# Performance work log

Measured on AMD Instinct MI355X. Metric: run time of the kernel, lower is better.

The kernel has to match this reference:

```python
import jax, jax.numpy as jnp
import numpy as np
from jax import lax

NUM_GROUPS = 16
POOL_K = 2
CLAMP_MIN = 0.0
CLAMP_MAX = 1.0
EPS = 1e-5


def setup_inputs() -> dict:
    key = jax.random.key(0)
    k1, k2, k3, k4, k5, k6 = jax.random.split(key, 6)
    B, Cin, H, W = 32, 64, 128, 128
    Cout, K = 128, 3
    x = jax.random.normal(k1, (B, Cin, H, W), dtype=jnp.float32)
    conv_w = jax.random.normal(k2, (Cout, Cin, K, K), dtype=jnp.float32) * 0.05
    conv_b = jax.random.normal(k3, (Cout,), dtype=jnp.float32) * 0.05
    gn_weight = jnp.ones((Cout,), dtype=jnp.float32) + 0.1 * jax.random.normal(k4, (Cout,), dtype=jnp.float32)
    gn_bias = 0.1 * jax.random.normal(k5, (Cout,), dtype=jnp.float32)
    scale = jnp.ones((Cout, 1, 1), dtype=jnp.float32) + 0.1 * jax.random.normal(k6, (Cout, 1, 1), dtype=jnp.float32)
    return {"x": x, "conv_w": conv_w, "conv_b": conv_b,
            "gn_weight": gn_weight, "gn_bias": gn_bias, "scale": scale}


def reference(x, conv_w, conv_b, gn_weight, gn_bias, scale):
    # Conv2d, VALID padding, stride 1  -> [B, C, H-2, W-2]
    y = lax.conv_general_dilated(
        x, conv_w, window_strides=(1, 1), padding='VALID',
        dimension_numbers=('NCHW', 'OIHW', 'NCHW'))
    y = y + conv_b[None, :, None, None]

    B, C, H, W = y.shape
    # GroupNorm: stats per (batch, group) over channels_per_group*H*W
    yg = y.reshape(B, NUM_GROUPS, -1)
    mean = jnp.mean(yg, axis=-1, keepdims=True)
    var = jnp.mean(jnp.square(yg - mean), axis=-1, keepdims=True)
    yn = ((yg - mean) * lax.rsqrt(var + EPS)).reshape(B, C, H, W)
    # affine + extra per-channel scale (fused elementwise)
    yn = (yn * gn_weight[None, :, None, None] + gn_bias[None, :, None, None]) * scale[None]

    # MaxPool2d(k=POOL_K), VALID, stride=k
    p = lax.reduce_window(yn, -jnp.inf, lax.max,
                          (1, 1, POOL_K, POOL_K), (1, 1, POOL_K, POOL_K), 'VALID')
    return jnp.clip(p, CLAMP_MIN, CLAMP_MAX)
```

## Files before the change

kernel.cpp:

```cpp
#include <hip/hip_runtime.h>

typedef _Float16 half8 __attribute__((ext_vector_type(8)));
typedef _Float16 half4t __attribute__((ext_vector_type(4)));
typedef _Float16 half2t __attribute__((ext_vector_type(2)));
typedef float float4t __attribute__((ext_vector_type(4)));
typedef float float4u __attribute__((ext_vector_type(4), aligned(4)));

#define BATCH 32
#define CIN 64
#define HIN 128
#define WIN 128
#define COUT 128
#define HOUT 126
#define WOUT 126
#define HP 63
#define WP 63
#define NGROUPS 16
#define CPG 8
#define EPSV 1e-5f

#define XPR 8320
#define XPRB 16640

__global__ __launch_bounds__(256) void wt_kernel(const float* __restrict__ w,
                                                 _Float16* __restrict__ wT) {
    int idx = blockIdx.x * 256 + threadIdx.x;
    if (idx >= 9 * COUT * CIN) return;
    int cin = idx & 63;
    int t = idx >> 6;
    int cout = t & 127;
    int pos = t >> 7;
    wT[idx] = (_Float16)w[(cout * CIN + cin) * 9 + pos];
}

__global__ __launch_bounds__(256) void repack_kernel(const float* __restrict__ x,
                                                     _Float16* __restrict__ xp) {
    __shared__ _Float16 lt[128 * 66];
    const int tid = threadIdx.x;
    const int grow = blockIdx.x;
    const int b = blockIdx.y;

    const int u = tid >> 5;
    const int col0 = (tid & 31) * 4;
    const float* xb = x + ((size_t)b * CIN * HIN + grow) * WIN;
#pragma unroll
    for (int i = 0; i < 4; i++) {
        int cin0 = 2 * (u + 8 * i);
        float4t va = *(const float4t*)(xb + (size_t)cin0 * HIN * WIN + col0);
        float4t vb = *(const float4t*)(xb + (size_t)(cin0 + 1) * HIN * WIN + col0);
#pragma unroll
        for (int j = 0; j < 4; j++) {
            half2t hv = { (_Float16)va[j], (_Float16)vb[j] };
            *(half2t*)&lt[(col0 + j) * 66 + cin0] = hv;
        }
    }
    __syncthreads();

    _Float16* xpb = xp + ((size_t)b * HIN + grow) * XPR;
#pragma unroll
    for (int k = 0; k < 16; k++) {
        int cidx = tid + 256 * k;
        int col = cidx >> 5, p = cidx & 31;
        half2t v = *(const half2t*)&lt[col * 66 + 2 * p];
        int slot = (p >> 2) ^ ((2 * grow + col) & 7);
        *(half2t*)(xpb + col * 64 + slot * 8 + (p & 3) * 2) = v;
    }
    if (tid < 16) {
        int col = 128 + (tid >> 3), chk = tid & 7;
        int slot = chk ^ ((2 * grow + col) & 7);
        half8 z;
#pragma unroll
        for (int j = 0; j < 8; j++) z[j] = (_Float16)0.f;
        *(half8*)(xpb + col * 64 + slot * 8) = z;
    }
}

__global__ __launch_bounds__(256, 2) void conv_mfma_kernel(
    const _Float16* __restrict__ xp, const _Float16* __restrict__ wT,
    const float* __restrict__ bias, unsigned int* __restrict__ pl,
    float* __restrict__ stats)
{
    __shared__ __align__(16) _Float16 xs[4 * XPR];

    const int tid = threadIdx.x;
    int f = blockIdx.y * 63 + blockIdx.x;
    int w = (f & 7) * 252 + (f >> 3);
    const int s = w % 63;
    const int b = w / 63;
    const int oy = 2 * s;

    const int lane = tid & 63;
    const int wv = tid >> 6;
    const int w2 = wv & 1;
    const int nh = wv >> 1;
    const int m = lane & 15;
    const int q = lane >> 4;
    const int cb = w2 * 64;

    {
        const char* src = (const char*)(xp + ((size_t)b * HIN + oy + wv) * XPR);
        char* dst = (char*)xs + wv * XPRB;
#pragma unroll
        for (int k = 0; k < 16; k++) {
            __builtin_amdgcn_global_load_lds(
                (const __attribute__((address_space(1))) void*)(src + k * 1024 + lane * 16),
                (__attribute__((address_space(3))) void*)(dst + k * 1024), 16, 0, 0);
        }
        __builtin_amdgcn_global_load_lds(
            (const __attribute__((address_space(1))) void*)(src + 16384 + lane * 4),
            (__attribute__((address_space(3))) void*)(dst + 16384), 4, 0, 0);
    }

    half8 a[4], na[4];
#pragma unroll
    for (int sub = 0; sub < 4; sub++)
        a[sub] = *(const half8*)(wT + ((size_t)(cb + sub * 16 + m)) * CIN + q * 8);

    float bv[4];
#pragma unroll
    for (int sub = 0; sub < 4; sub++) bv[sub] = bias[cb + sub * 16 + m];

    float4t acc0[4][4], acc1[4][4];
#pragma unroll
    for (int sub = 0; sub < 4; sub++)
#pragma unroll
        for (int n = 0; n < 4; n++) {
            acc0[sub][n] = (float4t){0.f, 0.f, 0.f, 0.f};
            acc1[sub][n] = (float4t){0.f, 0.f, 0.f, 0.f};
        }

    __syncthreads();

    for (int kk = 0; kk < 18; kk++) {
        int pos = kk >> 1, ch = kk & 1;
        int kh = (pos > 2) + (pos > 5);
        int kw = pos - kh * 3;
        int key0 = (2 * (oy + kh) + m + kw) & 7;
        int key1 = (key0 + 2) & 7;
        const _Float16* b0 = &xs[kh * XPR + (m + kw) * 64 + (((q + 4 * ch) ^ key0) << 3)];
        const _Float16* b1 = &xs[(kh + 1) * XPR + (m + kw) * 64 + (((q + 4 * ch) ^ key1) << 3)];

#pragma unroll
        for (int sub = 0; sub < 4; sub++) na[sub] = a[sub];
        if (kk < 17) {
            int nk = kk + 1, npos = nk >> 1, nch = nk & 1;
#pragma unroll
            for (int sub = 0; sub < 4; sub++)
                na[sub] = *(const half8*)(wT + ((size_t)(npos * COUT + cb + sub * 16 + m)) * CIN + q * 8 + nch * 32);
        }

#pragma unroll
        for (int n = 0; n < 4; n++) {
            half8 bf0 = *(const half8*)(b0 + (nh * 4 + n) * 1024);
            half8 bf1 = *(const half8*)(b1 + (nh * 4 + n) * 1024);
#pragma unroll
            for (int sub = 0; sub < 4; sub++) {
                acc0[sub][n] = __builtin_amdgcn_mfma_f32_16x16x32_f16(bf0, a[sub], acc0[sub][n], 0, 0, 0);
                acc1[sub][n] = __builtin_amdgcn_mfma_f32_16x16x32_f16(bf1, a[sub], acc1[sub][n], 0, 0, 0);
            }
        }
#pragma unroll
        for (int sub = 0; sub < 4; sub++) a[sub] = na[sub];
    }

    float sv[4] = {0.f, 0.f, 0.f, 0.f}, ssv[4] = {0.f, 0.f, 0.f, 0.f};
#pragma unroll
    for (int sub = 0; sub < 4; sub++) {
        const int c = cb + sub * 16 + m;
#pragma unroll
        for (int n = 0; n < 4; n++) {
            int pix0 = (nh * 4 + n) * 16 + q * 4;
            float p00 = acc0[sub][n][0] + bv[sub];
            float p01 = acc0[sub][n][1] + bv[sub];
            float p02 = acc0[sub][n][2] + bv[sub];
            float p03 = acc0[sub][n][3] + bv[sub];
            float p10 = acc1[sub][n][0] + bv[sub];
            float p11 = acc1[sub][n][1] + bv[sub];
            float p12 = acc1[sub][n][2] + bv[sub];
            float p13 = acc1[sub][n][3] + bv[sub];
            sv[sub]  += p00 + p01 + p10 + p11;
            ssv[sub] += p00 * p00 + p01 * p01 + p10 * p10 + p11 * p11;
            if (pix0 != 124) {
                sv[sub]  += p02 + p03 + p12 + p13;
                ssv[sub] += p02 * p02 + p03 * p03 + p12 * p12 + p13 * p13;
            }
            float mx0 = fmaxf(fmaxf(p00, p01), fmaxf(p10, p11));
            float mn0 = fminf(fminf(p00, p01), fminf(p10, p11));
            float mx1 = fmaxf(fmaxf(p02, p03), fmaxf(p12, p13));
            float mn1 = fminf(fminf(p02, p03), fminf(p12, p13));
            half4t o = { (_Float16)mx0, (_Float16)mn0, (_Float16)mx1, (_Float16)mn1 };
            unsigned int* dst = pl + (((size_t)b * COUT + c) * HP + s) * 64
                                + (nh * 4 + n) * 8 + 2 * q;
            *(half4t*)dst = o;
        }
    }

#pragma unroll
    for (int sub = 0; sub < 4; sub++) {
        float aa = sv[sub], cc = ssv[sub];
        aa += __shfl_xor(aa, 1);  cc += __shfl_xor(cc, 1);
        aa += __shfl_xor(aa, 2);  cc += __shfl_xor(cc, 2);
        aa += __shfl_xor(aa, 4);  cc += __shfl_xor(cc, 4);
        aa += __shfl_xor(aa, 16); cc += __shfl_xor(cc, 16);
        aa += __shfl_xor(aa, 32); cc += __shfl_xor(cc, 32);
        if ((lane & 55) == 0) {
            int g = w2 * 8 + sub * 2 + ((lane >> 3) & 1);
            atomicAdd(&stats[(b * NGROUPS + g) * 2 + 0], aa);
            atomicAdd(&stats[(b * NGROUPS + g) * 2 + 1], cc);
        }
    }
}

__global__ __launch_bounds__(256) void norm_pool_kernel(
    const unsigned int* __restrict__ pl, const float* __restrict__ stats,
    const float* __restrict__ gnw, const float* __restrict__ gnb,
    const float* __restrict__ scale, float* __restrict__ out)
{
    const int t  = threadIdx.x & 15;
    const int hs = threadIdx.x >> 4;
    const int hblk = blockIdx.x & 3;
    const int c = (blockIdx.x >> 2) & 127;
    const int b = blockIdx.x >> 9;
    const int hp = hblk * 16 + hs;

    const float N = (float)(CPG * HOUT * WOUT);
    int g = c >> 3;
    float sum   = stats[(b * NGROUPS + g) * 2 + 0];
    float sumsq = stats[(b * NGROUPS + g) * 2 + 1];
    float mean = sum / N;
    float var  = sumsq / N - mean * mean;
    float rstd = rsqrtf(var + EPSV);

    float gw = gnw[c] * rstd;
    float A  = gw * scale[c];
    float B2 = (gnb[c] - mean * gw) * scale[c];

    if (hp >= HP) return;

    const unsigned int* yp = pl + (((size_t)b * COUT + c) * HP + hp) * 64 + t * 4;
    half8 rv = *(const half8*)yp;

    float o[4];
#pragma unroll
    for (int j = 0; j < 4; j++) {
        float vx = fmaf((float)rv[2 * j],     A, B2);
        float vn = fmaf((float)rv[2 * j + 1], A, B2);
        float mx = fmaxf(vx, vn);
        o[j] = fminf(fmaxf(mx, 0.0f), 1.0f);
    }

    float* op = out + (((size_t)b * COUT + c) * HP + hp) * WP + t * 4;
    if (t < 15) {
        *(float4u*)op = (float4u){o[0], o[1], o[2], o[3]};
    } else {
        op[0] = o[0]; op[1] = o[1]; op[2] = o[2];
    }
}

extern "C" void kernel_launch(void* const* d_in, const int* in_sizes, int n_in,
                              void* d_out, int out_size, void* d_ws, size_t ws_size,
                              hipStream_t stream) {
    const float* x      = (const float*)d_in[0];
    const float* conv_w = (const float*)d_in[1];
    const float* conv_b = (const float*)d_in[2];
    const float* gnw    = (const float*)d_in[3];
    const float* gnb    = (const float*)d_in[4];
    const float* scale  = (const float*)d_in[5];
    float* out = (float*)d_out;

    const size_t pl_bytes = (size_t)BATCH * COUT * HP * 64 * 4;
    unsigned int* pl = (unsigned int*)d_ws;
    float* stats = (float*)((char*)d_ws + pl_bytes);
    _Float16* wT = (_Float16*)((char*)d_ws + pl_bytes + 4096);
    _Float16* xp = (_Float16*)((char*)d_ws + pl_bytes + 4096 + 147456);

    hipMemsetAsync(stats, 0, BATCH * NGROUPS * 2 * sizeof(float), stream);

    wt_kernel<<<(9 * COUT * CIN + 255) / 256, 256, 0, stream>>>(conv_w, wT);

    dim3 rgrid(HIN, BATCH);
    repack_kernel<<<rgrid, 256, 0, stream>>>(x, xp);

    dim3 grid(HP, BATCH);
    conv_mfma_kernel<<<grid, 256, 0, stream>>>(xp, wT, conv_b, pl, stats);

    norm_pool_kernel<<<BATCH * COUT * 4, 256, 0, stream>>>(
        pl, stats, gnw, gnb, scale, out);
}
```

Baseline: 365.1 us.

## Split conv output rows across 512-thread blocks and widen repack stores

The conv kernel now uses 512 threads per block, with each wave computing a single output row instead of two. The two rows' max/min partials are combined through LDS before the store. This halves the accumulator registers per thread and the launch bounds now request higher occupancy, at the cost of an extra LDS exchange and two barriers. Weight prefetching is replaced by per-iteration loads, and the repack kernel switches to padded LDS rows and 16-byte vector stores.

```diff
diff --git a/kernel.cpp b/kernel.cpp
--- a/kernel.cpp
+++ b/kernel.cpp
@@ -35,7 +35,7 @@
 
 __global__ __launch_bounds__(256) void repack_kernel(const float* __restrict__ x,
                                                      _Float16* __restrict__ xp) {
-    __shared__ _Float16 lt[128 * 66];
+    __shared__ _Float16 lt[128 * 72];
     const int tid = threadIdx.x;
     const int grow = blockIdx.x;
     const int b = blockIdx.y;
@@ -51,19 +51,19 @@
 #pragma unroll
         for (int j = 0; j < 4; j++) {
             half2t hv = { (_Float16)va[j], (_Float16)vb[j] };
-            *(half2t*)&lt[(col0 + j) * 66 + cin0] = hv;
+            *(half2t*)&lt[(col0 + j) * 72 + cin0] = hv;
         }
     }
     __syncthreads();
 
     _Float16* xpb = xp + ((size_t)b * HIN + grow) * XPR;
 #pragma unroll
-    for (int k = 0; k < 16; k++) {
+    for (int k = 0; k < 4; k++) {
         int cidx = tid + 256 * k;
-        int col = cidx >> 5, p = cidx & 31;
-        half2t v = *(const half2t*)&lt[col * 66 + 2 * p];
-        int slot = (p >> 2) ^ ((2 * grow + col) & 7);
-        *(half2t*)(xpb + col * 64 + slot * 8 + (p & 3) * 2) = v;
+        int col = cidx >> 3, chk = cidx & 7;
+        half8 v = *(const half8*)&lt[col * 72 + chk * 8];
+        int slot = chk ^ ((2 * grow + col) & 7);
+        *(half8*)(xpb + col * 64 + slot * 8) = v;
     }
     if (tid < 16) {
         int col = 128 + (tid >> 3), chk = tid & 7;
@@ -75,7 +75,7 @@
     }
 }
 
-__global__ __launch_bounds__(256, 2) void conv_mfma_kernel(
+__global__ __launch_bounds__(512, 4) void conv_mfma_kernel(
     const _Float16* __restrict__ xp, const _Float16* __restrict__ wT,
     const float* __restrict__ bias, unsigned int* __restrict__ pl,
     float* __restrict__ stats)
@@ -92,106 +92,114 @@
     const int lane = tid & 63;
     const int wv = tid >> 6;
     const int w2 = wv & 1;
-    const int nh = wv >> 1;
+    const int nh = (wv >> 1) & 1;
+    const int row = wv >> 2;
     const int m = lane & 15;
     const int q = lane >> 4;
     const int cb = w2 * 64;
 
     {
-        const char* src = (const char*)(xp + ((size_t)b * HIN + oy + wv) * XPR);
-        char* dst = (char*)xs + wv * XPRB;
-#pragma unroll
-        for (int k = 0; k < 16; k++) {
+        const char* src = (const char*)(xp + ((size_t)b * HIN + oy) * XPR);
+#pragma unroll
+        for (int k = 0; k < 8; k++) {
+            int chunk = wv * 8 + k;
             __builtin_amdgcn_global_load_lds(
-                (const __attribute__((address_space(1))) void*)(src + k * 1024 + lane * 16),
-                (__attribute__((address_space(3))) void*)(dst + k * 1024), 16, 0, 0);
-        }
-        __builtin_amdgcn_global_load_lds(
-            (const __attribute__((address_space(1))) void*)(src + 16384 + lane * 4),
-            (__attribute__((address_space(3))) void*)(dst + 16384), 4, 0, 0);
-    }
-
-    half8 a[4], na[4];
+                (const __attribute__((address_space(1))) void*)(src + chunk * 1024 + lane * 16),
+                (__attribute__((address_space(3))) void*)((char*)xs + chunk * 1024), 16, 0, 0);
+        }
+        if (wv == 0) {
+            __builtin_amdgcn_global_load_lds(
+                (const __attribute__((address_space(1))) void*)(src + 65536 + lane * 16),
+                (__attribute__((address_space(3))) void*)((char*)xs + 65536), 16, 0, 0);
+        }
+    }
+
+    float bv[4];
+#pragma unroll
+    for (int sub = 0; sub < 4; sub++) bv[sub] = bias[cb + sub * 16 + m];
+
+    float4t acc[4][4];
 #pragma unroll
     for (int sub = 0; sub < 4; sub++)
-        a[sub] = *(const half8*)(wT + ((size_t)(cb + sub * 16 + m)) * CIN + q * 8);
-
-    float bv[4];
-#pragma unroll
-    for (int sub = 0; sub < 4; sub++) bv[sub] = bias[cb + sub * 16 + m];
-
-    float4t acc0[4][4], acc1[4][4];
-#pragma unroll
-    for (int sub = 0; sub < 4; sub++)
+#pragma unroll
+        for (int n = 0; n < 4; n++)
+            acc[sub][n] = (float4t){0.f, 0.f, 0.f, 0.f};
+
+    __syncthreads();
+
+    const int r = oy + row;
+#pragma unroll
+    for (int kk = 0; kk < 18; kk++) {
+        const int pos = kk >> 1, ch = kk & 1;
+        const int kh = (pos > 2) + (pos > 5);
+        const int kw = pos - kh * 3;
+        int key = (2 * (r + kh) + m + kw) & 7;
+        const _Float16* bb = &xs[(row + kh) * XPR + (m + kw) * 64 + (((q + 4 * ch) ^ key) << 3)];
+
+        half8 aw[4];
+#pragma unroll
+        for (int sub = 0; sub < 4; sub++)
+            aw[sub] = *(const half8*)(wT + ((size_t)(pos * COUT + cb + sub * 16 + m)) * CIN + q * 8 + ch * 32);
+
 #pragma unroll
         for (int n = 0; n < 4; n++) {
-            acc0[sub][n] = (float4t){0.f, 0.f, 0.f, 0.f};
-            acc1[sub][n] = (float4t){0.f, 0.f, 0.f, 0.f};
-        }
-
-    __syncthreads();
-
-    for (int kk = 0; kk < 18; kk++) {
-        int pos = kk >> 1, ch = kk & 1;
-        int kh = (pos > 2) + (pos > 5);
-        int kw = pos - kh * 3;
-        int key0 = (2 * (oy + kh) + m + kw) & 7;
-        int key1 = (key0 + 2) & 7;
-        const _Float16* b0 = &xs[kh * XPR + (m + kw) * 64 + (((q + 4 * ch) ^ key0) << 3)];
-        const _Float16* b1 = &xs[(kh + 1) * XPR + (m + kw) * 64 + (((q + 4 * ch) ^ key1) << 3)];
-
-#pragma unroll
-        for (int sub = 0; sub < 4; sub++) na[sub] = a[sub];
-        if (kk < 17) {
-            int nk = kk + 1, npos = nk >> 1, nch = nk & 1;
+            half8 bf = *(const half8*)(bb + (nh * 4 + n) * 1024);
 #pragma unroll
             for (int sub = 0; sub < 4; sub++)
-                na[sub] = *(const half8*)(wT + ((size_t)(npos * COUT + cb + sub * 16 + m)) * CIN + q * 8 + nch * 32);
-        }
-
-#pragma unroll
-        for (int n = 0; n < 4; n++) {
-            half8 bf0 = *(const half8*)(b0 + (nh * 4 + n) * 1024);
-            half8 bf1 = *(const half8*)(b1 + (nh * 4 + n) * 1024);
-#pragma unroll
-            for (int sub = 0; sub < 4; sub++) {
-                acc0[sub][n] = __builtin_amdgcn_mfma_f32_16x16x32_f16(bf0, a[sub], acc0[sub][n], 0, 0, 0);
-                acc1[sub][n] = __builtin_amdgcn_mfma_f32_16x16x32_f16(bf1, a[sub], acc1[sub][n], 0, 0, 0);
-            }
-        }
-#pragma unroll
-        for (int sub = 0; sub < 4; sub++) a[sub] = na[sub];
+                acc[sub][n] = __builtin_amdgcn_mfma_f32_16x16x32_f16(bf, aw[sub], acc[sub][n], 0, 0, 0);
+        }
     }
 
     float sv[4] = {0.f, 0.f, 0.f, 0.f}, ssv[4] = {0.f, 0.f, 0.f, 0.f};
+    half4t hmm[4][4];
 #pragma unroll
     for (int sub = 0; sub < 4; sub++) {
-        const int c = cb + sub * 16 + m;
 #pragma unroll
         for (int n = 0; n < 4; n++) {
             int pix0 = (nh * 4 + n) * 16 + q * 4;
-            float p00 = acc0[sub][n][0] + bv[sub];
-            float p01 = acc0[sub][n][1] + bv[sub];
-            float p02 = acc0[sub][n][2] + bv[sub];
-            float p03 = acc0[sub][n][3] + bv[sub];
-            float p10 = acc1[sub][n][0] + bv[sub];
-            float p11 = acc1[sub][n][1] + bv[sub];
-            float p12 = acc1[sub][n][2] + bv[sub];
-            float p13 = acc1[sub][n][3] + bv[sub];
-            sv[sub]  += p00 + p01 + p10 + p11;
-            ssv[sub] += p00 * p00 + p01 * p01 + p10 * p10 + p11 * p11;
+            float p0 = acc[sub][n][0] + bv[sub];
+            float p1 = acc[sub][n][1] + bv[sub];
+            float p2 = acc[sub][n][2] + bv[sub];
+            float p3 = acc[sub][n][3] + bv[sub];
+            sv[sub]  += p0 + p1;
+            ssv[sub] += p0 * p0 + p1 * p1;
             if (pix0 != 124) {
-                sv[sub]  += p02 + p03 + p12 + p13;
-                ssv[sub] += p02 * p02 + p03 * p03 + p12 * p12 + p13 * p13;
+                sv[sub]  += p2 + p3;
+                ssv[sub] += p2 * p2 + p3 * p3;
             }
-            float mx0 = fmaxf(fmaxf(p00, p01), fmaxf(p10, p11));
-            float mn0 = fminf(fminf(p00, p01), fminf(p10, p11));
-            float mx1 = fmaxf(fmaxf(p02, p03), fmaxf(p12, p13));
-            float mn1 = fminf(fminf(p02, p03), fminf(p12, p13));
-            half4t o = { (_Float16)mx0, (_Float16)mn0, (_Float16)mx1, (_Float16)mn1 };
-            unsigned int* dst = pl + (((size_t)b * COUT + c) * HP + s) * 64
-                                + (nh * 4 + n) * 8 + 2 * q;
-            *(half4t*)dst = o;
+            float mx0 = fmaxf(p0, p1), mn0 = fminf(p0, p1);
+            float mx1 = fmaxf(p2, p3), mn1 = fminf(p2, p3);
+            hmm[sub][n] = (half4t){ (_Float16)mx0, (_Float16)mn0,
+                                    (_Float16)mx1, (_Float16)mn1 };
+        }
+    }
+
+    __syncthreads();
+    half4t* sc = (half4t*)xs;
+    if (row == 1) {
+#pragma unroll
+        for (int sub = 0; sub < 4; sub++)
+#pragma unroll
+            for (int n = 0; n < 4; n++)
+                sc[(((wv & 3) * 4 + sub) * 4 + n) * 64 + lane] = hmm[sub][n];
+    }
+    __syncthreads();
+    if (row == 0) {
+#pragma unroll
+        for (int sub = 0; sub < 4; sub++) {
+            const int c = cb + sub * 16 + m;
+#pragma unroll
+            for (int n = 0; n < 4; n++) {
+                half4t o2 = sc[(((wv & 3) * 4 + sub) * 4 + n) * 64 + lane];
+                half4t h = hmm[sub][n];
+                half4t o = { h[0] > o2[0] ? h[0] : o2[0],
+                             h[1] < o2[1] ? h[1] : o2[1],
+                             h[2] > o2[2] ? h[2] : o2[2],
+                             h[3] < o2[3] ? h[3] : o2[3] };
+                unsigned int* dst = pl + (((size_t)b * COUT + c) * HP + s) * 64
+                                    + (nh * 4 + n) * 8 + 2 * q;
+                *(half4t*)dst = o;
+            }
         }
     }
 
@@ -282,7 +290,7 @@
     repack_kernel<<<rgrid, 256, 0, stream>>>(x, xp);
 
     dim3 grid(HP, BATCH);
-    conv_mfma_kernel<<<grid, 256, 0, stream>>>(xp, wT, conv_b, pl, stats);
+    conv_mfma_kernel<<<grid, 512, 0, stream>>>(xp, wT, conv_b, pl, stats);
 
     norm_pool_kernel<<<BATCH * COUT * 4, 256, 0, stream>>>(
         pl, stats, gnw, gnb, scale, out);
```

New measurement: 430.7 us. 1.18x slower.

## Fuse weight transpose, stats zeroing and input repack into one prep kernel

Applied to the files above, without the earlier changes.

Merges the memset, weight transpose kernel and input repack kernel into a single launch, with extra blocks handling the weight transpose and stats zeroing. The repack now does the transpose in registers instead of through shared memory, with each thread writing whole 16-byte half8 chunks. The conv kernel's global-to-LDS copy is restructured so that all four waves share one contiguous copy of the four rows, replacing a 4-byte tail load with one 16-byte load. This removes two launches and an LDS round trip, at the cost of less coalesced loads: each thread reads eight separate channel planes.

```diff
diff --git a/kernel.cpp b/kernel.cpp
--- a/kernel.cpp
+++ b/kernel.cpp
@@ -22,52 +22,47 @@
 #define XPR 8320
 #define XPRB 16640
 
-__global__ __launch_bounds__(256) void wt_kernel(const float* __restrict__ w,
-                                                 _Float16* __restrict__ wT) {
-    int idx = blockIdx.x * 256 + threadIdx.x;
-    if (idx >= 9 * COUT * CIN) return;
-    int cin = idx & 63;
-    int t = idx >> 6;
-    int cout = t & 127;
-    int pos = t >> 7;
-    wT[idx] = (_Float16)w[(cout * CIN + cin) * 9 + pos];
-}
-
-__global__ __launch_bounds__(256) void repack_kernel(const float* __restrict__ x,
-                                                     _Float16* __restrict__ xp) {
-    __shared__ _Float16 lt[128 * 66];
+__global__ __launch_bounds__(256) void prep_kernel(
+    const float* __restrict__ x, const float* __restrict__ w,
+    _Float16* __restrict__ xp, _Float16* __restrict__ wT,
+    float* __restrict__ stats)
+{
     const int tid = threadIdx.x;
+    if (blockIdx.x >= 128) {
+        const int pos = blockIdx.x - 128;
+        const int idx = blockIdx.y * 256 + tid;
+        const int cout = idx >> 6, cin = idx & 63;
+        wT[pos * (COUT * CIN) + idx] = (_Float16)w[(cout * CIN + cin) * 9 + pos];
+        if (blockIdx.x == 128 && blockIdx.y == 0)
+            ((float4t*)stats)[tid] = (float4t){0.f, 0.f, 0.f, 0.f};
+        return;
+    }
+
     const int grow = blockIdx.x;
     const int b = blockIdx.y;
-
-    const int u = tid >> 5;
-    const int col0 = (tid & 31) * 4;
-    const float* xb = x + ((size_t)b * CIN * HIN + grow) * WIN;
-#pragma unroll
-    for (int i = 0; i < 4; i++) {
-        int cin0 = 2 * (u + 8 * i);
-        float4t va = *(const float4t*)(xb + (size_t)cin0 * HIN * WIN + col0);
-        float4t vb = *(const float4t*)(xb + (size_t)(cin0 + 1) * HIN * WIN + col0);
-#pragma unroll
-        for (int j = 0; j < 4; j++) {
-            half2t hv = { (_Float16)va[j], (_Float16)vb[j] };
-            *(half2t*)&lt[(col0 + j) * 66 + cin0] = hv;
-        }
-    }
-    __syncthreads();
+    const int colq = tid >> 3;
+    const int chk  = tid & 7;
+    const int c0 = colq * 4;
+
+    const float* xb = x + (((size_t)b * CIN + chk * 8) * HIN + grow) * WIN + c0;
+    float4t v[8];
+#pragma unroll
+    for (int i = 0; i < 8; i++)
+        v[i] = *(const float4t*)(xb + (size_t)i * HIN * WIN);
 
     _Float16* xpb = xp + ((size_t)b * HIN + grow) * XPR;
 #pragma unroll
-    for (int k = 0; k < 16; k++) {
-        int cidx = tid + 256 * k;
-        int col = cidx >> 5, p = cidx & 31;
-        half2t v = *(const half2t*)&lt[col * 66 + 2 * p];
-        int slot = (p >> 2) ^ ((2 * grow + col) & 7);
-        *(half2t*)(xpb + col * 64 + slot * 8 + (p & 3) * 2) = v;
+    for (int j = 0; j < 4; j++) {
+        int col = c0 + j;
+        int slot = chk ^ ((2 * grow + col) & 7);
+        half8 h = { (_Float16)v[0][j], (_Float16)v[1][j], (_Float16)v[2][j],
+                    (_Float16)v[3][j], (_Float16)v[4][j], (_Float16)v[5][j],
+                    (_Float16)v[6][j], (_Float16)v[7][j] };
+        *(half8*)(xpb + col * 64 + slot * 8) = h;
     }
     if (tid < 16) {
-        int col = 128 + (tid >> 3), chk = tid & 7;
-        int slot = chk ^ ((2 * grow + col) & 7);
+        int col = 128 + (tid >> 3), ck = tid & 7;
+        int slot = ck ^ ((2 * grow + col) & 7);
         half8 z;
 #pragma unroll
         for (int j = 0; j < 8; j++) z[j] = (_Float16)0.f;
@@ -98,17 +93,19 @@
     const int cb = w2 * 64;
 
     {
-        const char* src = (const char*)(xp + ((size_t)b * HIN + oy + wv) * XPR);
-        char* dst = (char*)xs + wv * XPRB;
+        const char* src = (const char*)(xp + ((size_t)b * HIN + oy) * XPR);
 #pragma unroll
         for (int k = 0; k < 16; k++) {
+            int chunk = wv * 16 + k;
             __builtin_amdgcn_global_load_lds(
-                (const __attribute__((address_space(1))) void*)(src + k * 1024 + lane * 16),
-                (__attribute__((address_space(3))) void*)(dst + k * 1024), 16, 0, 0);
-        }
-        __builtin_amdgcn_global_load_lds(
-            (const __attribute__((address_space(1))) void*)(src + 16384 + lane * 4),
-            (__attribute__((address_space(3))) void*)(dst + 16384), 4, 0, 0);
+                (const __attribute__((address_space(1))) void*)(src + chunk * 1024 + lane * 16),
+                (__attribute__((address_space(3))) void*)((char*)xs + chunk * 1024), 16, 0, 0);
+        }
+        if (wv == 0) {
+            __builtin_amdgcn_global_load_lds(
+                (const __attribute__((address_space(1))) void*)(src + 65536 + lane * 16),
+                (__attribute__((address_space(3))) void*)((char*)xs + 65536), 16, 0, 0);
+        }
     }
 
     half8 a[4], na[4];
@@ -274,12 +271,8 @@
     _Float16* wT = (_Float16*)((char*)d_ws + pl_bytes + 4096);
     _Float16* xp = (_Float16*)((char*)d_ws + pl_bytes + 4096 + 147456);
 
-    hipMemsetAsync(stats, 0, BATCH * NGROUPS * 2 * sizeof(float), stream);
-
-    wt_kernel<<<(9 * COUT * CIN + 255) / 256, 256, 0, stream>>>(conv_w, wT);
-
-    dim3 rgrid(HIN, BATCH);
-    repack_kernel<<<rgrid, 256, 0, stream>>>(x, xp);
+    dim3 pgrid(137, BATCH);
+    prep_kernel<<<pgrid, 256, 0, stream>>>(x, conv_w, xp, wT, stats);
 
     dim3 grid(HP, BATCH);
     conv_mfma_kernel<<<grid, 256, 0, stream>>>(xp, wT, conv_b, pl, stats);
```

New measurement: 362.9 us. About the same (-0.6%).
